# Kernel tuning notes

Measured on AMD Instinct MI355X. Metric: run time of the kernel, lower is better.

## Reference

```python
import jax, jax.numpy as jnp
import numpy as np

EPS = 1e-5

def _conv(x, w, b):
    # NCHW x OIHW -> NCHW, stride 1, SAME padding (stencil center (1,1) of 3x3, or 1x1)
    y = jax.lax.conv_general_dilated(x, w, (1, 1), 'SAME',
                                     dimension_numbers=('NCHW', 'OIHW', 'NCHW'))
    return y + b[None, :, None, None]

def _bn(x, gamma, beta):
    # training-mode batchnorm: stats over (N, H, W) per channel
    mean = jnp.mean(x, axis=(0, 2, 3), keepdims=True)
    var = jnp.var(x, axis=(0, 2, 3), keepdims=True)
    xhat = (x - mean) * jax.lax.rsqrt(var + EPS)
    return xhat * gamma[None, :, None, None] + beta[None, :, None, None]

def setup_inputs() -> dict:
    key = jax.random.key(0)
    ks = jax.random.split(key, 12)
    B, Cin, Cout, H, W = 2, 64, 64, 512, 512
    s = 0.05
    return {
        'x':  jax.random.normal(ks[0], (B, Cin, H, W), jnp.float32),
        'w1': jax.random.normal(ks[1], (Cout, Cin, 3, 3), jnp.float32) * s,
        'b1': jnp.zeros((Cout,), jnp.float32),
        'g1': jnp.ones((Cout,), jnp.float32),
        'be1': jnp.zeros((Cout,), jnp.float32),
        'w2': jax.random.normal(ks[2], (Cout, Cout, 3, 3), jnp.float32) * s,
        'b2': jnp.zeros((Cout,), jnp.float32),
        'g2': jnp.ones((Cout,), jnp.float32),
        'be2': jnp.zeros((Cout,), jnp.float32),
        'wp': jax.random.normal(ks[3], (Cout, Cin, 1, 1), jnp.float32) * s,
        'bp': jnp.zeros((Cout,), jnp.float32),
        'gp': jnp.ones((Cout,), jnp.float32),
        'bep': jnp.zeros((Cout,), jnp.float32),
    }

def reference(x, w1, b1, g1, be1, w2, b2, g2, be2, wp, bp, gp, bep):
    # project branch: 1x1 conv ([(0,0)] stencil) + BN
    residual = _bn(_conv(x, wp, bp), gp, bep)
    # conv1: pad + 3x3 lattice conv (full cp stencil) + BN + Identity downsample + ReLU
    out = jax.nn.relu(_bn(_conv(x, w1, b1), g1, be1))
    # conv2: pad + 3x3 lattice conv + BN
    out = _bn(_conv(out, w2, b2), g2, be2)
    # residual add + output ReLU
    return jax.nn.relu(out + residual)
```

## Files before the change

kernel.cpp:

```cpp
#include <hip/hip_runtime.h>
#include <hip/hip_bf16.h>
#include <stdint.h>

typedef short short8 __attribute__((ext_vector_type(8)));
typedef float f32x4 __attribute__((ext_vector_type(4)));
typedef unsigned int u32;
typedef unsigned short u16;

#define HH 512
#define WW 512
#define CC 64
#define PLANE (HH*WW)
#define NSTATF 524288.0f

#define KTW 32
#define HSTR 560
#define KBSTR 1120
#define SLOTB 4480
#define NSLOT 8
#define RINGB (NSLOT*SLOTB)
#define BOUNCEB 16384
#define NBC 1024
#define K5S 260

__device__ __forceinline__ u16 f2bf(float f) {
  __hip_bfloat16 h = __float2bfloat16(f);
  return __builtin_bit_cast(u16, h);
}
__device__ __forceinline__ u32 pk2bf(float a, float b) {
  return (u32)f2bf(a) | ((u32)f2bf(b) << 16);
}
__device__ __forceinline__ float bf2f(u16 u) {
  u32 x = ((u32)u) << 16;
  return __builtin_bit_cast(float, x);
}
__device__ __forceinline__ void lds_barrier() {
  asm volatile("s_waitcnt lgkmcnt(0)" ::: "memory");
  __builtin_amdgcn_s_barrier();
  __builtin_amdgcn_sched_barrier(0);
}

__global__ __launch_bounds__(512) void kprep(const float* __restrict__ w1,
    const float* __restrict__ w2, const float* __restrict__ wp,
    u16* __restrict__ wb1, u16* __restrict__ wb2, u16* __restrict__ wbp)
{
  const int id = blockIdx.x*512 + threadIdx.x;
  const int lane = id & 63;
  if (id < 9216) {
    const float* w = (id < 4608) ? w1 : w2;
    u16* o = (id < 4608) ? wb1 : wb2;
    const int fid = (id < 4608) ? (id >> 6) : ((id - 4608) >> 6);
    const int ct4 = fid / 18, rem = fid % 18;
    const int tap = rem >> 1, kb = rem & 1;
    const int cout = ct4*16 + (lane & 15);
    const int k0c = kb*32 + (lane >> 4)*8;
    u32 ow[4];
#pragma unroll
    for (int p = 0; p < 4; ++p) {
      float a = w[(size_t)(cout*64 + k0c + p*2    )*9 + tap];
      float b = w[(size_t)(cout*64 + k0c + p*2 + 1)*9 + tap];
      ow[p] = pk2bf(a, b);
    }
    *(uint4*)(o + ((size_t)fid*64 + lane)*8) = make_uint4(ow[0],ow[1],ow[2],ow[3]);
  } else if (id < 9728) {
    const int fid = (id - 9216) >> 6;
    const int ct4 = fid >> 1, kb = fid & 1;
    const int cout = ct4*16 + (lane & 15);
    const int k0c = kb*32 + (lane >> 4)*8;
    u32 ow[4];
#pragma unroll
    for (int p = 0; p < 4; ++p)
      ow[p] = pk2bf(wp[cout*64 + k0c + p*2], wp[cout*64 + k0c + p*2 + 1]);
    *(uint4*)(wbp + ((size_t)fid*64 + lane)*8) = make_uint4(ow[0],ow[1],ow[2],ow[3]);
  }
}

__global__ __launch_bounds__(256) void k0(const float* __restrict__ x, u16* __restrict__ xh)
{
  __shared__ __align__(16) u32 Tp[32*260];
  const int tid = threadIdx.x;
  const int wt = blockIdx.x, h = blockIdx.y, n = blockIdx.z;
  const int w0 = wt*256;
  const float* xp = x + (size_t)n*CC*PLANE + (size_t)h*WW + w0;
#pragma unroll
  for (int it = 0; it < 8; ++it) {
    const int j = it*256 + tid;
    const int c2 = j >> 6, w4 = (j & 63) << 2;
    const f32x4 a = *(const f32x4*)(xp + (size_t)(c2*2    )*PLANE + w4);
    const f32x4 b = *(const f32x4*)(xp + (size_t)(c2*2 + 1)*PLANE + w4);
    uint4 o;
    o.x = pk2bf(a[0], b[0]);
    o.y = pk2bf(a[1], b[1]);
    o.z = pk2bf(a[2], b[2]);
    o.w = pk2bf(a[3], b[3]);
    *(uint4*)(Tp + (u32)c2*260 + (u32)(w4 ^ (4*(c2 >> 2)))) = o;
  }
  __syncthreads();
  u16* op = xh + ((size_t)(n*HH + h)*WW + w0)*CC;
#pragma unroll
  for (int it = 0; it < 8; ++it) {
    const int j = it*256 + tid;
    const int w = j >> 3, c8 = j & 7;
    const u32 wsw = (u32)(w ^ (4*c8));
    uint4 o;
    o.x = Tp[(u32)(c8*4 + 0)*260 + wsw];
    o.y = Tp[(u32)(c8*4 + 1)*260 + wsw];
    o.z = Tp[(u32)(c8*4 + 2)*260 + wsw];
    o.w = Tp[(u32)(c8*4 + 3)*260 + wsw];
    *(uint4*)(op + (size_t)w*CC + c8*8) = o;
  }
}

template<bool BNS, bool PROJ>
__global__ __launch_bounds__(256, 2) void kconv(const u16* __restrict__ in,
    const u16* __restrict__ wb, const u16* __restrict__ wbp,
    const float* __restrict__ As, const float* __restrict__ Bs,
    u16* __restrict__ out, u16* __restrict__ yp,
    float* __restrict__ ps, float* __restrict__ pq,
    float* __restrict__ psp, float* __restrict__ pqp)
{
  __shared__ __align__(16) char LB[RINGB + BOUNCEB + 512];
  float* sA = (float*)(LB + RINGB + BOUNCEB);
  float* sB = sA + 64;
  const int tid = threadIdx.x;
  const int lane = tid & 63, wv = tid >> 6;
  const int l15 = lane & 15, lq = lane >> 4;
  const int wt = blockIdx.x, hs = blockIdx.y, n = blockIdx.z;
  const int w0 = wt*KTW, h0 = hs*16;
  const int bid = (n*32 + hs)*16 + wt;

  if (BNS) {
    if (tid < 64) { sA[tid] = As[tid]; sB[tid] = Bs[tid]; }
    __syncthreads();
  }

  short8 wfr[18];
#pragma unroll
  for (int f = 0; f < 18; ++f)
    wfr[f] = *(const short8*)(wb + ((size_t)(wv*18 + f)*64 + lane)*8);
  short8 wpf[2];
  if constexpr (PROJ) {
#pragma unroll
    for (int kb = 0; kb < 2; ++kb)
      wpf[kb] = *(const short8*)(wbp + ((size_t)(wv*2 + kb)*64 + lane)*8);
  }

  float s4[4] = {0,0,0,0}, q4[4] = {0,0,0,0};
  float sp4[4] = {0,0,0,0}, qp4[4] = {0,0,0,0};
  const u16* inb = in + (size_t)n*PLANE*CC;
  const u32 co0 = (u32)((lq >> 1)*KBSTR + (lq & 1)*HSTR);
  const u32 co1 = co0 + 2*KBSTR;

  auto ld_one = [&](int j, int cl, int c8) -> uint4 {
    const int gh = h0 - 1 + j, gw = w0 - 1 + cl;
    if (((u32)gh < (u32)HH) && ((u32)gw < (u32)WW))
      return *(const uint4*)(inb + ((size_t)gh*WW + gw)*CC + c8*8);
    return make_uint4(0u,0u,0u,0u);
  };
  auto st_one = [&](int slot, int cl, int c8, uint4 v) {
    if (BNS) {
      const u32* uw = (const u32*)&v;
      u32 ow[4];
      const int cb = c8*8;
#pragma unroll
      for (int h2 = 0; h2 < 4; ++h2) {
        float f0 = fmaxf(bf2f((u16)(uw[h2] & 0xFFFFu)) * sA[cb+h2*2]   + sB[cb+h2*2],   0.f);
        float f1 = fmaxf(bf2f((u16)(uw[h2] >> 16))     * sA[cb+h2*2+1] + sB[cb+h2*2+1], 0.f);
        ow[h2] = pk2bf(f0, f1);
      }
      v = make_uint4(ow[0],ow[1],ow[2],ow[3]);
    }
    *(uint4*)(LB + (size_t)slot*SLOTB + (c8>>1)*KBSTR + (c8&1)*HSTR + cl*16) = v;
  };

  for (int idx = tid; idx < 4*272; idx += 256) {
    const int jj = idx / 272, rem = idx - jj*272;
    st_one(jj, rem >> 3, rem & 7, ld_one(jj, rem >> 3, rem & 7));
  }
  __syncthreads();

  uint4 st0, st1, st2;
  auto issue2 = [&](int jb) {
    { const int idx = tid;       const int jj = idx/272, rem = idx - jj*272;
      st0 = ld_one(jb + jj, rem >> 3, rem & 7); }
    { const int idx = 256 + tid; const int jj = idx/272, rem = idx - jj*272;
      st1 = ld_one(jb + jj, rem >> 3, rem & 7); }
    if (tid < 32) { const int idx = 512 + tid; const int jj = idx/272, rem = idx - jj*272;
      st2 = ld_one(jb + jj, rem >> 3, rem & 7); }
  };
  auto write2 = [&](int jb) {
    { const int idx = tid;       const int jj = idx/272, rem = idx - jj*272;
      st_one((jb + jj) & 7, rem >> 3, rem & 7, st0); }
    { const int idx = 256 + tid; const int jj = idx/272, rem = idx - jj*272;
      st_one((jb + jj) & 7, rem >> 3, rem & 7, st1); }
    if (tid < 32) { const int idx = 512 + tid; const int jj = idx/272, rem = idx - jj*272;
      st_one((jb + jj) & 7, rem >> 3, rem & 7, st2); }
  };

  issue2(4);

  for (int g = 0; g < 8; ++g) {
    if (g > 0) write2(2*g + 2);
    lds_barrier();
    if (g < 7) issue2(2*g + 4);

    const char* sb[4];
#pragma unroll
    for (int mi = 0; mi < 4; ++mi)
      sb[mi] = LB + (size_t)((2*g + mi) & 7)*SLOTB + l15*16;
    f32x4 a0t0, a0t1, a1t0, a1t1;
    f32x4 p0t0, p0t1, p1t0, p1t1;
#pragma unroll
    for (int r = 0; r < 4; ++r) {
      a0t0[r]=0.f; a0t1[r]=0.f; a1t0[r]=0.f; a1t1[r]=0.f;
      p0t0[r]=0.f; p0t1[r]=0.f; p1t0[r]=0.f; p1t1[r]=0.f;
    }
#pragma unroll
    for (int t = 0; t < 2; ++t) {
      const int pb = t*16;
#pragma unroll
      for (int kb = 0; kb < 2; ++kb) {
        const u32 ck = kb ? co1 : co0;
#pragma unroll
        for (int mi = 0; mi < 4; ++mi) {
#pragma unroll
          for (int kw = 0; kw < 3; ++kw) {
            const short8 X = *(const short8*)(sb[mi] + ck + (u32)((pb + kw)*16));
            if (mi <= 2) {
              const short8 Wf = wfr[(mi*3 + kw)*2 + kb];
              if (t == 0) a0t0 = __builtin_amdgcn_mfma_f32_16x16x32_bf16(Wf, X, a0t0, 0,0,0);
              else        a0t1 = __builtin_amdgcn_mfma_f32_16x16x32_bf16(Wf, X, a0t1, 0,0,0);
            }
            if (mi >= 1) {
              const short8 Wf = wfr[((mi-1)*3 + kw)*2 + kb];
              if (t == 0) a1t0 = __builtin_amdgcn_mfma_f32_16x16x32_bf16(Wf, X, a1t0, 0,0,0);
              else        a1t1 = __builtin_amdgcn_mfma_f32_16x16x32_bf16(Wf, X, a1t1, 0,0,0);
            }
            if constexpr (PROJ) {
              if (kw == 1 && mi == 1) {
                if (t == 0) p0t0 = __builtin_amdgcn_mfma_f32_16x16x32_bf16(wpf[kb], X, p0t0, 0,0,0);
                else        p0t1 = __builtin_amdgcn_mfma_f32_16x16x32_bf16(wpf[kb], X, p0t1, 0,0,0);
              }
              if (kw == 1 && mi == 2) {
                if (t == 0) p1t0 = __builtin_amdgcn_mfma_f32_16x16x32_bf16(wpf[kb], X, p1t0, 0,0,0);
                else        p1t1 = __builtin_amdgcn_mfma_f32_16x16x32_bf16(wpf[kb], X, p1t1, 0,0,0);
              }
            }
          }
        }
      }
    }
    {
      const int co = wv*16 + lq*4;
#pragma unroll
      for (int r = 0; r < 4; ++r) {
        s4[r] += a0t0[r] + a0t1[r] + a1t0[r] + a1t1[r];
        q4[r] = fmaf(a0t0[r], a0t0[r], q4[r]);
        q4[r] = fmaf(a0t1[r], a0t1[r], q4[r]);
        q4[r] = fmaf(a1t0[r], a1t0[r], q4[r]);
        q4[r] = fmaf(a1t1[r], a1t1[r], q4[r]);
      }
      if constexpr (PROJ) {
#pragma unroll
        for (int r = 0; r < 4; ++r) {
          sp4[r] += p0t0[r] + p0t1[r] + p1t0[r] + p1t1[r];
          qp4[r] = fmaf(p0t0[r], p0t0[r], qp4[r]);
          qp4[r] = fmaf(p0t1[r], p0t1[r], qp4[r]);
          qp4[r] = fmaf(p1t0[r], p1t0[r], qp4[r]);
          qp4[r] = fmaf(p1t1[r], p1t1[r], qp4[r]);
        }
      }
#pragma unroll
      for (int t = 0; t < 2; ++t) {
        const int pos = t*16 + l15;
        const u32 addr = ((u32)(pos*128 + co*2)) ^ (((u32)(pos & 7)) << 4);
        uint2 c0, c1;
        if (t == 0) {
          c0.x = pk2bf(a0t0[0], a0t0[1]); c0.y = pk2bf(a0t0[2], a0t0[3]);
          c1.x = pk2bf(a1t0[0], a1t0[1]); c1.y = pk2bf(a1t0[2], a1t0[3]);
        } else {
          c0.x = pk2bf(a0t1[0], a0t1[1]); c0.y = pk2bf(a0t1[2], a0t1[3]);
          c1.x = pk2bf(a1t1[0], a1t1[1]); c1.y = pk2bf(a1t1[2], a1t1[3]);
        }
        *(uint2*)(LB + RINGB + 0*4096 + addr) = c0;
        *(uint2*)(LB + RINGB + 1*4096 + addr) = c1;
        if constexpr (PROJ) {
          uint2 d0, d1;
          if (t == 0) {
            d0.x = pk2bf(p0t0[0], p0t0[1]); d0.y = pk2bf(p0t0[2], p0t0[3]);
            d1.x = pk2bf(p1t0[0], p1t0[1]); d1.y = pk2bf(p1t0[2], p1t0[3]);
          } else {
            d0.x = pk2bf(p0t1[0], p0t1[1]); d0.y = pk2bf(p0t1[2], p0t1[3]);
            d1.x = pk2bf(p1t1[0], p1t1[1]); d1.y = pk2bf(p1t1[2], p1t1[3]);
          }
          *(uint2*)(LB + RINGB + 2*4096 + addr) = d0;
          *(uint2*)(LB + RINGB + 3*4096 + addr) = d1;
        }
      }
    }
    lds_barrier();
    if constexpr (PROJ) {
      const int rowi = tid >> 6, tt = tid & 63;
      const int pos = tt >> 1, half = (tt & 1)*64;
      const char* bb = LB + RINGB + rowi*4096;
      u16* base = (rowi < 2) ? out : yp;
      const int orow = h0 + 2*g + (rowi & 1);
      char* dst = (char*)base + ((size_t)((n*HH + orow)*WW + w0 + pos))*128 + half;
      const u32 sw = ((u32)(pos & 7)) << 4;
#pragma unroll
      for (int k2 = 0; k2 < 4; ++k2) {
        const uint4 v = *(const uint4*)(bb + (((u32)(pos*128 + half + k2*16)) ^ sw));
        *(uint4*)(dst + k2*16) = v;
      }
    } else {
      const int rowi = tid >> 7, tt = tid & 127;
      const int pos = tt >> 2, qb = (tt & 3)*32;
      const char* bb = LB + RINGB + rowi*4096;
      const u32 a0 = ((u32)(pos*128 + qb)) ^ (((u32)(pos & 7)) << 4);
      const uint4 v0 = *(const uint4*)(bb + a0);
      const uint4 v1 = *(const uint4*)(bb + (a0 ^ 16u));
      char* dst = (char*)out + ((size_t)((n*HH + h0 + 2*g + rowi)*WW + w0 + pos))*128 + qb;
      *(uint4*)dst = v0;
      *(uint4*)(dst + 16) = v1;
    }
  }

#pragma unroll
  for (int d = 1; d <= 8; d <<= 1) {
#pragma unroll
    for (int r = 0; r < 4; ++r) {
      s4[r] += __shfl_xor(s4[r], d, 64);
      q4[r] += __shfl_xor(q4[r], d, 64);
    }
  }
  if (l15 == 0) {
#pragma unroll
    for (int r = 0; r < 4; ++r) {
      const int co = wv*16 + lq*4 + r;
      ps[(size_t)co*NBC + bid] = s4[r];
      pq[(size_t)co*NBC + bid] = q4[r];
    }
  }
  if constexpr (PROJ) {
#pragma unroll
    for (int d = 1; d <= 8; d <<= 1) {
#pragma unroll
      for (int r = 0; r < 4; ++r) {
        sp4[r] += __shfl_xor(sp4[r], d, 64);
        qp4[r] += __shfl_xor(qp4[r], d, 64);
      }
    }
    if (l15 == 0) {
#pragma unroll
      for (int r = 0; r < 4; ++r) {
        const int co = wv*16 + lq*4 + r;
        psp[(size_t)co*NBC + bid] = sp4[r];
        pqp[(size_t)co*NBC + bid] = qp4[r];
      }
    }
  }
}

__global__ __launch_bounds__(256) void kfin2(
    const float* __restrict__ psA, const float* __restrict__ pqA,
    const float* __restrict__ gA, const float* __restrict__ beA,
    float* __restrict__ AA, float* __restrict__ BA, int cntA,
    const float* __restrict__ psB, const float* __restrict__ pqB,
    const float* __restrict__ gB, const float* __restrict__ beB,
    float* __restrict__ AB, float* __restrict__ BB, int cntB)
{
  const int blk = blockIdx.x;
  const bool second = blk >= 64;
  const int c = blk & 63;
  const float* psx = second ? psB : psA;
  const float* pqx = second ? pqB : pqA;
  const float* g  = second ? gB  : gA;
  const float* be = second ? beB : beA;
  float* A  = second ? AB : AA;
  float* Bc = second ? BB : BA;
  const int cnt = second ? cntB : cntA;

  const int t = threadIdx.x;
  float sv = 0.f, s2 = 0.f;
  const float* pr = psx + (size_t)c*cnt;
  const float* qr = pqx + (size_t)c*cnt;
  for (int k = t; k < cnt; k += 256) { sv += pr[k]; s2 += qr[k]; }
#pragma unroll
  for (int d = 1; d < 64; d <<= 1) { sv += __shfl_xor(sv, d, 64); s2 += __shfl_xor(s2, d, 64); }
  __shared__ float as_[4], aq_[4];
  if ((t & 63) == 0) { as_[t >> 6] = sv; aq_[t >> 6] = s2; }
  __syncthreads();
  if (t == 0) {
    sv = as_[0] + as_[1] + as_[2] + as_[3];
    s2 = aq_[0] + aq_[1] + aq_[2] + aq_[3];
    const float mean = sv / NSTATF;
    const float var = s2 / NSTATF - mean*mean;
    const float istd = rsqrtf(var + 1e-5f);
    const float a = g[c] * istd;
    A[c] = a;
    Bc[c] = be[c] - mean * a;
  }
}

__global__ __launch_bounds__(256) void k5(const u16* __restrict__ y2, const u16* __restrict__ yp,
    const float* __restrict__ A2, const float* __restrict__ B2c,
    const float* __restrict__ Ap, const float* __restrict__ Bp,
    float* __restrict__ outp)
{
  __shared__ float T[CC*K5S];
  __shared__ float cA2[64], cB2[64], cAp[64], cBp[64];
  const int tid = threadIdx.x;
  const int lane = tid & 63, wv = tid >> 6;
  const int wt = blockIdx.x, h = blockIdx.y, n = blockIdx.z;
  const int w0 = wt*256;
  if (tid < 64) { cA2[tid] = A2[tid]; cB2[tid] = B2c[tid]; cAp[tid] = Ap[tid]; cBp[tid] = Bp[tid]; }
  __syncthreads();
  const u16* p2 = y2 + ((size_t)(n*HH + h)*WW + w0)*CC;
  const u16* pp = yp + ((size_t)(n*HH + h)*WW + w0)*CC;
#pragma unroll
  for (int it = 0; it < 8; ++it) {
    const int j = it*256 + tid;
    const int w = j >> 3, c8 = j & 7;
    const uint4 u2 = *(const uint4*)(p2 + (size_t)w*CC + c8*8);
    const uint4 up = *(const uint4*)(pp + (size_t)w*CC + c8*8);
    const u32* m2 = (const u32*)&u2;
    const u32* mp = (const u32*)&up;
    const u32 sw = ((u32)(c8 & 3)) << 3;
#pragma unroll
    for (int h2 = 0; h2 < 4; ++h2) {
      const int c = c8*8 + h2*2;
      const float a = bf2f((u16)(m2[h2] & 0xFFFFu)), b = bf2f((u16)(m2[h2] >> 16));
      const float ra = bf2f((u16)(mp[h2] & 0xFFFFu)), rb = bf2f((u16)(mp[h2] >> 16));
      const u32 wsw = (u32)w ^ sw;
      T[(u32)(c    )*K5S + wsw] = fmaxf(a*cA2[c]   + cB2[c]   + ra*cAp[c]   + cBp[c],   0.f);
      T[(u32)(c + 1)*K5S + wsw] = fmaxf(b*cA2[c+1] + cB2[c+1] + rb*cAp[c+1] + cBp[c+1], 0.f);
    }
  }
  __syncthreads();
#pragma unroll
  for (int cc = 0; cc < 16; ++cc) {
    const int c = cc*4 + wv;
    const u32 sw = ((u32)((c >> 3) & 3)) << 3;
    const u32 idx = (u32)c*K5S + (((u32)lane*4) ^ sw);
    const f32x4 v = *(const f32x4*)(T + idx);
    *(f32x4*)(outp + ((size_t)((n*CC + c)*HH + h))*WW + w0 + lane*4) = v;
  }
}

extern "C" void kernel_launch(void* const* d_in, const int* in_sizes, int n_in,
                              void* d_out, int out_size, void* d_ws, size_t ws_size,
                              hipStream_t stream)
{
  (void)in_sizes; (void)n_in; (void)out_size;
  const float* x   = (const float*)d_in[0];
  const float* w1  = (const float*)d_in[1];
  const float* g1  = (const float*)d_in[3];
  const float* be1 = (const float*)d_in[4];
  const float* w2  = (const float*)d_in[5];
  const float* g2  = (const float*)d_in[7];
  const float* be2 = (const float*)d_in[8];
  const float* wp  = (const float*)d_in[9];
  const float* gp  = (const float*)d_in[11];
  const float* bep = (const float*)d_in[12];

  const size_t TENB = (size_t)2*CC*PLANE*2;
  char* ws = (char*)d_ws;
  u16* bufA = (u16*)ws;
  u16* bufB = (u16*)(ws + TENB);
  u16* bufC = (u16*)(ws + TENB*2);
  char* aux = ws + TENB*3;
  u16* wb1 = (u16*)aux;
  u16* wb2 = (u16*)(aux + 73728);
  u16* wbp = (u16*)(aux + 147456);
  float* ps1 = (float*)(aux + 155648);
  float* pq1 = ps1 + 64*NBC;
  float* ps2 = pq1 + 64*NBC;
  float* pq2 = ps2 + 64*NBC;
  float* psp = pq2 + 64*NBC;
  float* pqp = psp + 64*NBC;
  float* A1  = pqp + 64*NBC;
  float* B1  = A1 + 64;
  float* A2  = B1 + 64;
  float* B2c = A2 + 64;
  float* Ap  = B2c + 64;
  float* Bp  = Ap + 64;
  const size_t need = (size_t)(Bp + 64 - (float*)ws) * 4;
  if (ws_size < need) return;

  kprep<<<19, 512, 0, stream>>>(w1, w2, wp, wb1, wb2, wbp);
  k0<<<dim3(2, HH, 2), 256, 0, stream>>>(x, bufA);
  kconv<false, true><<<dim3(16, 32, 2), 256, 0, stream>>>(bufA, wb1, wbp, nullptr, nullptr,
                                                          bufB, bufC, ps1, pq1, psp, pqp);
  kfin2<<<128, 256, 0, stream>>>(ps1, pq1, g1, be1, A1, B1, NBC,
                                 psp, pqp, gp, bep, Ap, Bp, NBC);
  kconv<true, false><<<dim3(16, 32, 2), 256, 0, stream>>>(bufB, wb2, nullptr, A1, B1,
                                                          bufA, nullptr, ps2, pq2, nullptr, nullptr);
  kfin2<<<64, 256, 0, stream>>>(ps2, pq2, g2, be2, A2, B2c, NBC,
                                ps2, pq2, g2, be2, A2, B2c, NBC);
  k5<<<dim3(2, HH, 2), 256, 0, stream>>>(bufA, bufC, A2, B2c, Ap, Bp, (float*)d_out);
}
```

Baseline: 223.5 us.

## Rewrite second conv with 32x32 MFMA tiles and deeper staging ring

Splits the templated conv kernel into a specialised conv1 (with fused projection) and a new conv2. Conv2 uses 32x32x16 bf16 MFMA with each wave owning 32 output channels and two output rows, and a 10-slot LDS ring staging four rows per step. The goal is better MFMA throughput and fewer barrier steps per block. It costs more registers, since 36 weight fragments and 16-wide accumulators are held per wave, which may hurt occupancy. The final epilogue kernel also moves to half-width tiles, doubling its grid and using float2 stores.

```diff
diff --git a/kernel.cpp b/kernel.cpp
--- a/kernel.cpp
+++ b/kernel.cpp
@@ -4,6 +4,7 @@
 
 typedef short short8 __attribute__((ext_vector_type(8)));
 typedef float f32x4 __attribute__((ext_vector_type(4)));
+typedef float f32x16 __attribute__((ext_vector_type(16)));
 typedef unsigned int u32;
 typedef unsigned short u16;
 
@@ -14,14 +15,19 @@
 #define NSTATF 524288.0f
 
 #define KTW 32
-#define HSTR 560
-#define KBSTR 1120
-#define SLOTB 4480
-#define NSLOT 8
-#define RINGB (NSLOT*SLOTB)
+#define HSTR1 560
+#define KBSTR1 1120
+#define SLOTB1 4480
+#define RING1 (8*SLOTB1)
+#define HSTR2 592
+#define KBSTR2 1184
+#define SLOTB2 4736
+#define NSLOT2 10
+#define RING2 (NSLOT2*SLOTB2)
 #define BOUNCEB 16384
-#define NBC 1024
-#define K5S 260
+#define NBC1 1024
+#define NBC2 2048
+#define K5S 132
 
 __device__ __forceinline__ u16 f2bf(float f) {
   __hip_bfloat16 h = __float2bfloat16(f);
@@ -46,10 +52,8 @@
 {
   const int id = blockIdx.x*512 + threadIdx.x;
   const int lane = id & 63;
-  if (id < 9216) {
-    const float* w = (id < 4608) ? w1 : w2;
-    u16* o = (id < 4608) ? wb1 : wb2;
-    const int fid = (id < 4608) ? (id >> 6) : ((id - 4608) >> 6);
+  if (id < 4608) {
+    const int fid = id >> 6;
     const int ct4 = fid / 18, rem = fid % 18;
     const int tap = rem >> 1, kb = rem & 1;
     const int cout = ct4*16 + (lane & 15);
@@ -57,11 +61,23 @@
     u32 ow[4];
 #pragma unroll
     for (int p = 0; p < 4; ++p) {
-      float a = w[(size_t)(cout*64 + k0c + p*2    )*9 + tap];
-      float b = w[(size_t)(cout*64 + k0c + p*2 + 1)*9 + tap];
-      ow[p] = pk2bf(a, b);
-    }
-    *(uint4*)(o + ((size_t)fid*64 + lane)*8) = make_uint4(ow[0],ow[1],ow[2],ow[3]);
+      ow[p] = pk2bf(w1[(size_t)(cout*64 + k0c + p*2)*9 + tap],
+                    w1[(size_t)(cout*64 + k0c + p*2 + 1)*9 + tap]);
+    }
+    *(uint4*)(wb1 + ((size_t)fid*64 + lane)*8) = make_uint4(ow[0],ow[1],ow[2],ow[3]);
+  } else if (id < 9216) {
+    const int fid = (id - 4608) >> 6;
+    const int ct = fid / 36, rem = fid % 36;
+    const int tap = rem >> 2, kb = rem & 3;
+    const int cout = ct*32 + (lane & 31);
+    const int cinb = kb*16 + (lane >> 5)*8;
+    u32 ow[4];
+#pragma unroll
+    for (int p = 0; p < 4; ++p) {
+      ow[p] = pk2bf(w2[(size_t)(cout*64 + cinb + p*2)*9 + tap],
+                    w2[(size_t)(cout*64 + cinb + p*2 + 1)*9 + tap]);
+    }
+    *(uint4*)(wb2 + ((size_t)fid*64 + lane)*8) = make_uint4(ow[0],ow[1],ow[2],ow[3]);
   } else if (id < 9728) {
     const int fid = (id - 9216) >> 6;
     const int ct4 = fid >> 1, kb = fid & 1;
@@ -111,17 +127,13 @@
   }
 }
 
-template<bool BNS, bool PROJ>
-__global__ __launch_bounds__(256, 2) void kconv(const u16* __restrict__ in,
+__global__ __launch_bounds__(256, 2) void kconv1(const u16* __restrict__ in,
     const u16* __restrict__ wb, const u16* __restrict__ wbp,
-    const float* __restrict__ As, const float* __restrict__ Bs,
     u16* __restrict__ out, u16* __restrict__ yp,
     float* __restrict__ ps, float* __restrict__ pq,
     float* __restrict__ psp, float* __restrict__ pqp)
 {
-  __shared__ __align__(16) char LB[RINGB + BOUNCEB + 512];
-  float* sA = (float*)(LB + RINGB + BOUNCEB);
-  float* sB = sA + 64;
+  __shared__ __align__(16) char LB[RING1 + BOUNCEB + 512];
   const int tid = threadIdx.x;
   const int lane = tid & 63, wv = tid >> 6;
   const int l15 = lane & 15, lq = lane >> 4;
@@ -129,27 +141,20 @@
   const int w0 = wt*KTW, h0 = hs*16;
   const int bid = (n*32 + hs)*16 + wt;
 
-  if (BNS) {
-    if (tid < 64) { sA[tid] = As[tid]; sB[tid] = Bs[tid]; }
-    __syncthreads();
-  }
-
   short8 wfr[18];
 #pragma unroll
   for (int f = 0; f < 18; ++f)
     wfr[f] = *(const short8*)(wb + ((size_t)(wv*18 + f)*64 + lane)*8);
   short8 wpf[2];
-  if constexpr (PROJ) {
-#pragma unroll
-    for (int kb = 0; kb < 2; ++kb)
-      wpf[kb] = *(const short8*)(wbp + ((size_t)(wv*2 + kb)*64 + lane)*8);
-  }
+#pragma unroll
+  for (int kb = 0; kb < 2; ++kb)
+    wpf[kb] = *(const short8*)(wbp + ((size_t)(wv*2 + kb)*64 + lane)*8);
 
   float s4[4] = {0,0,0,0}, q4[4] = {0,0,0,0};
   float sp4[4] = {0,0,0,0}, qp4[4] = {0,0,0,0};
   const u16* inb = in + (size_t)n*PLANE*CC;
-  const u32 co0 = (u32)((lq >> 1)*KBSTR + (lq & 1)*HSTR);
-  const u32 co1 = co0 + 2*KBSTR;
+  const u32 co0 = (u32)((lq >> 1)*KBSTR1 + (lq & 1)*HSTR1);
+  const u32 co1 = co0 + 2*KBSTR1;
 
   auto ld_one = [&](int j, int cl, int c8) -> uint4 {
     const int gh = h0 - 1 + j, gw = w0 - 1 + cl;
@@ -158,19 +163,7 @@
     return make_uint4(0u,0u,0u,0u);
   };
   auto st_one = [&](int slot, int cl, int c8, uint4 v) {
-    if (BNS) {
-      const u32* uw = (const u32*)&v;
-      u32 ow[4];
-      const int cb = c8*8;
-#pragma unroll
-      for (int h2 = 0; h2 < 4; ++h2) {
-        float f0 = fmaxf(bf2f((u16)(uw[h2] & 0xFFFFu)) * sA[cb+h2*2]   + sB[cb+h2*2],   0.f);
-        float f1 = fmaxf(bf2f((u16)(uw[h2] >> 16))     * sA[cb+h2*2+1] + sB[cb+h2*2+1], 0.f);
-        ow[h2] = pk2bf(f0, f1);
-      }
-      v = make_uint4(ow[0],ow[1],ow[2],ow[3]);
-    }
-    *(uint4*)(LB + (size_t)slot*SLOTB + (c8>>1)*KBSTR + (c8&1)*HSTR + cl*16) = v;
+    *(uint4*)(LB + (size_t)slot*SLOTB1 + (c8>>1)*KBSTR1 + (c8&1)*HSTR1 + cl*16) = v;
   };
 
   for (int idx = tid; idx < 4*272; idx += 256) {
@@ -207,7 +200,7 @@
     const char* sb[4];
 #pragma unroll
     for (int mi = 0; mi < 4; ++mi)
-      sb[mi] = LB + (size_t)((2*g + mi) & 7)*SLOTB + l15*16;
+      sb[mi] = LB + (size_t)((2*g + mi) & 7)*SLOTB1 + l15*16;
     f32x4 a0t0, a0t1, a1t0, a1t1;
     f32x4 p0t0, p0t1, p1t0, p1t1;
 #pragma unroll
@@ -236,15 +229,13 @@
               if (t == 0) a1t0 = __builtin_amdgcn_mfma_f32_16x16x32_bf16(Wf, X, a1t0, 0,0,0);
               else        a1t1 = __builtin_amdgcn_mfma_f32_16x16x32_bf16(Wf, X, a1t1, 0,0,0);
             }
-            if constexpr (PROJ) {
-              if (kw == 1 && mi == 1) {
-                if (t == 0) p0t0 = __builtin_amdgcn_mfma_f32_16x16x32_bf16(wpf[kb], X, p0t0, 0,0,0);
-                else        p0t1 = __builtin_amdgcn_mfma_f32_16x16x32_bf16(wpf[kb], X, p0t1, 0,0,0);
-              }
-              if (kw == 1 && mi == 2) {
-                if (t == 0) p1t0 = __builtin_amdgcn_mfma_f32_16x16x32_bf16(wpf[kb], X, p1t0, 0,0,0);
-                else        p1t1 = __builtin_amdgcn_mfma_f32_16x16x32_bf16(wpf[kb], X, p1t1, 0,0,0);
-              }
+            if (kw == 1 && mi == 1) {
+              if (t == 0) p0t0 = __builtin_amdgcn_mfma_f32_16x16x32_bf16(wpf[kb], X, p0t0, 0,0,0);
+              else        p0t1 = __builtin_amdgcn_mfma_f32_16x16x32_bf16(wpf[kb], X, p0t1, 0,0,0);
+            }
+            if (kw == 1 && mi == 2) {
+              if (t == 0) p1t0 = __builtin_amdgcn_mfma_f32_16x16x32_bf16(wpf[kb], X, p1t0, 0,0,0);
+              else        p1t1 = __builtin_amdgcn_mfma_f32_16x16x32_bf16(wpf[kb], X, p1t1, 0,0,0);
             }
           }
         }
@@ -259,50 +250,39 @@
         q4[r] = fmaf(a0t1[r], a0t1[r], q4[r]);
         q4[r] = fmaf(a1t0[r], a1t0[r], q4[r]);
         q4[r] = fmaf(a1t1[r], a1t1[r], q4[r]);
-      }
-      if constexpr (PROJ) {
-#pragma unroll
-        for (int r = 0; r < 4; ++r) {
-          sp4[r] += p0t0[r] + p0t1[r] + p1t0[r] + p1t1[r];
-          qp4[r] = fmaf(p0t0[r], p0t0[r], qp4[r]);
-          qp4[r] = fmaf(p0t1[r], p0t1[r], qp4[r]);
-          qp4[r] = fmaf(p1t0[r], p1t0[r], qp4[r]);
-          qp4[r] = fmaf(p1t1[r], p1t1[r], qp4[r]);
-        }
+        sp4[r] += p0t0[r] + p0t1[r] + p1t0[r] + p1t1[r];
+        qp4[r] = fmaf(p0t0[r], p0t0[r], qp4[r]);
+        qp4[r] = fmaf(p0t1[r], p0t1[r], qp4[r]);
+        qp4[r] = fmaf(p1t0[r], p1t0[r], qp4[r]);
+        qp4[r] = fmaf(p1t1[r], p1t1[r], qp4[r]);
       }
 #pragma unroll
       for (int t = 0; t < 2; ++t) {
         const int pos = t*16 + l15;
         const u32 addr = ((u32)(pos*128 + co*2)) ^ (((u32)(pos & 7)) << 4);
-        uint2 c0, c1;
+        uint2 c0, c1, d0, d1;
         if (t == 0) {
           c0.x = pk2bf(a0t0[0], a0t0[1]); c0.y = pk2bf(a0t0[2], a0t0[3]);
           c1.x = pk2bf(a1t0[0], a1t0[1]); c1.y = pk2bf(a1t0[2], a1t0[3]);
+          d0.x = pk2bf(p0t0[0], p0t0[1]); d0.y = pk2bf(p0t0[2], p0t0[3]);
+          d1.x = pk2bf(p1t0[0], p1t0[1]); d1.y = pk2bf(p1t0[2], p1t0[3]);
         } else {
           c0.x = pk2bf(a0t1[0], a0t1[1]); c0.y = pk2bf(a0t1[2], a0t1[3]);
           c1.x = pk2bf(a1t1[0], a1t1[1]); c1.y = pk2bf(a1t1[2], a1t1[3]);
+          d0.x = pk2bf(p0t1[0], p0t1[1]); d0.y = pk2bf(p0t1[2], p0t1[3]);
+          d1.x = pk2bf(p1t1[0], p1t1[1]); d1.y = pk2bf(p1t1[2], p1t1[3]);
         }
-        *(uint2*)(LB + RINGB + 0*4096 + addr) = c0;
-        *(uint2*)(LB + RINGB + 1*4096 + addr) = c1;
-        if constexpr (PROJ) {
-          uint2 d0, d1;
-          if (t == 0) {
-            d0.x = pk2bf(p0t0[0], p0t0[1]); d0.y = pk2bf(p0t0[2], p0t0[3]);
-            d1.x = pk2bf(p1t0[0], p1t0[1]); d1.y = pk2bf(p1t0[2], p1t0[3]);
-          } else {
-            d0.x = pk2bf(p0t1[0], p0t1[1]); d0.y = pk2bf(p0t1[2], p0t1[3]);
-            d1.x = pk2bf(p1t1[0], p1t1[1]); d1.y = pk2bf(p1t1[2], p1t1[3]);
-          }
-          *(uint2*)(LB + RINGB + 2*4096 + addr) = d0;
-          *(uint2*)(LB + RINGB + 3*4096 + addr) = d1;
-        }
+        *(uint2*)(LB + RING1 + 0*4096 + addr) = c0;
+        *(uint2*)(LB + RING1 + 1*4096 + addr) = c1;
+        *(uint2*)(LB + RING1 + 2*4096 + addr) = d0;
+        *(uint2*)(LB + RING1 + 3*4096 + addr) = d1;
       }
     }
     lds_barrier();
-    if constexpr (PROJ) {
+    {
       const int rowi = tid >> 6, tt = tid & 63;
       const int pos = tt >> 1, half = (tt & 1)*64;
-      const char* bb = LB + RINGB + rowi*4096;
+      const char* bb = LB + RING1 + rowi*4096;
       u16* base = (rowi < 2) ? out : yp;
       const int orow = h0 + 2*g + (rowi & 1);
       char* dst = (char*)base + ((size_t)((n*HH + orow)*WW + w0 + pos))*128 + half;
@@ -312,16 +292,6 @@
         const uint4 v = *(const uint4*)(bb + (((u32)(pos*128 + half + k2*16)) ^ sw));
         *(uint4*)(dst + k2*16) = v;
       }
-    } else {
-      const int rowi = tid >> 7, tt = tid & 127;
-      const int pos = tt >> 2, qb = (tt & 3)*32;
-      const char* bb = LB + RINGB + rowi*4096;
-      const u32 a0 = ((u32)(pos*128 + qb)) ^ (((u32)(pos & 7)) << 4);
-      const uint4 v0 = *(const uint4*)(bb + a0);
-      const uint4 v1 = *(const uint4*)(bb + (a0 ^ 16u));
-      char* dst = (char*)out + ((size_t)((n*HH + h0 + 2*g + rowi)*WW + w0 + pos))*128 + qb;
-      *(uint4*)dst = v0;
-      *(uint4*)(dst + 16) = v1;
     }
   }
 
@@ -331,32 +301,190 @@
     for (int r = 0; r < 4; ++r) {
       s4[r] += __shfl_xor(s4[r], d, 64);
       q4[r] += __shfl_xor(q4[r], d, 64);
+      sp4[r] += __shfl_xor(sp4[r], d, 64);
+      qp4[r] += __shfl_xor(qp4[r], d, 64);
     }
   }
   if (l15 == 0) {
 #pragma unroll
     for (int r = 0; r < 4; ++r) {
       const int co = wv*16 + lq*4 + r;
-      ps[(size_t)co*NBC + bid] = s4[r];
-      pq[(size_t)co*NBC + bid] = q4[r];
-    }
-  }
-  if constexpr (PROJ) {
-#pragma unroll
-    for (int d = 1; d <= 8; d <<= 1) {
-#pragma unroll
-      for (int r = 0; r < 4; ++r) {
-        sp4[r] += __shfl_xor(sp4[r], d, 64);
-        qp4[r] += __shfl_xor(qp4[r], d, 64);
-      }
-    }
-    if (l15 == 0) {
-#pragma unroll
-      for (int r = 0; r < 4; ++r) {
-        const int co = wv*16 + lq*4 + r;
-        psp[(size_t)co*NBC + bid] = sp4[r];
-        pqp[(size_t)co*NBC + bid] = qp4[r];
-      }
+      ps[(size_t)co*NBC1 + bid] = s4[r];
+      pq[(size_t)co*NBC1 + bid] = q4[r];
+      psp[(size_t)co*NBC1 + bid] = sp4[r];
+      pqp[(size_t)co*NBC1 + bid] = qp4[r];
+    }
+  }
+}
+
+__global__ __launch_bounds__(256, 2) void kconv2(const u16* __restrict__ in,
+    const u16* __restrict__ wb,
+    const float* __restrict__ As, const float* __restrict__ Bs,
+    u16* __restrict__ out, float* __restrict__ ps, float* __restrict__ pq)
+{
+  __shared__ __align__(16) char LB[RING2 + BOUNCEB + 512];
+  float* sA = (float*)(LB + RING2 + BOUNCEB);
+  float* sB = sA + 64;
+  const int tid = threadIdx.x;
+  const int lane = tid & 63, wv = tid >> 6;
+  const int ct = wv & 1, ro = wv >> 1;
+  const int wt = blockIdx.x, hs = blockIdx.y, n = blockIdx.z;
+  const int w0 = wt*KTW, h0 = hs*16;
+  const int bid = (n*32 + hs)*16 + wt;
+
+  if (tid < 64) { sA[tid] = As[tid]; sB[tid] = Bs[tid]; }
+  __syncthreads();
+
+  short8 wfr[36];
+#pragma unroll
+  for (int f = 0; f < 36; ++f)
+    wfr[f] = *(const short8*)(wb + ((size_t)(ct*36 + f)*64 + lane)*8);
+  float s[16], q[16];
+#pragma unroll
+  for (int r = 0; r < 16; ++r) { s[r] = 0.f; q[r] = 0.f; }
+
+  const u16* inb = in + (size_t)n*PLANE*CC;
+  const u32 lt = (u32)((lane & 31)*16 + (lane >> 5)*HSTR2);
+
+  auto ld_one = [&](int j, int cl, int c8) -> uint4 {
+    const int gh = h0 - 1 + j, gw = w0 - 1 + cl;
+    if (((u32)gh < (u32)HH) && ((u32)gw < (u32)WW))
+      return *(const uint4*)(inb + ((size_t)gh*WW + gw)*CC + c8*8);
+    return make_uint4(0u,0u,0u,0u);
+  };
+  auto st_one = [&](int slot, int cl, int c8, uint4 v) {
+    const u32* uw = (const u32*)&v;
+    u32 ow[4];
+    const int cb = c8*8;
+#pragma unroll
+    for (int h2 = 0; h2 < 4; ++h2) {
+      float f0 = fmaxf(bf2f((u16)(uw[h2] & 0xFFFFu)) * sA[cb+h2*2]   + sB[cb+h2*2],   0.f);
+      float f1 = fmaxf(bf2f((u16)(uw[h2] >> 16))     * sA[cb+h2*2+1] + sB[cb+h2*2+1], 0.f);
+      ow[h2] = pk2bf(f0, f1);
+    }
+    *(uint4*)(LB + (size_t)slot*SLOTB2 + (c8>>1)*KBSTR2 + (c8&1)*HSTR2 + cl*16) =
+        make_uint4(ow[0],ow[1],ow[2],ow[3]);
+  };
+
+  for (int idx = tid; idx < 6*272; idx += 256) {
+    const int jj = idx / 272, rem = idx - jj*272;
+    st_one(jj, rem >> 3, rem & 7, ld_one(jj, rem >> 3, rem & 7));
+  }
+  __syncthreads();
+
+  for (int g = 0; g < 4; ++g) {
+    const bool dostage = (g <= 2);
+    const int jb = 4*g + 6;
+    uint4 st0, st1, st2, st3, st4;
+    if (dostage) {
+      { const int idx = tid;        const int jj = idx/272, rem = idx - jj*272;
+        st0 = ld_one(jb + jj, rem >> 3, rem & 7); }
+      { const int idx = 256 + tid;  const int jj = idx/272, rem = idx - jj*272;
+        st1 = ld_one(jb + jj, rem >> 3, rem & 7); }
+      { const int idx = 512 + tid;  const int jj = idx/272, rem = idx - jj*272;
+        st2 = ld_one(jb + jj, rem >> 3, rem & 7); }
+      { const int idx = 768 + tid;  const int jj = idx/272, rem = idx - jj*272;
+        st3 = ld_one(jb + jj, rem >> 3, rem & 7); }
+      if (tid < 64) { const int idx = 1024 + tid; const int jj = idx/272, rem = idx - jj*272;
+        st4 = ld_one(jb + jj, rem >> 3, rem & 7); }
+    }
+
+    const int r0 = 4*g + 2*ro;
+    f32x16 acc0, acc1;
+#pragma unroll
+    for (int rr = 0; rr < 16; ++rr) { acc0[rr] = 0.f; acc1[rr] = 0.f; }
+    {
+      const char* bm[4];
+#pragma unroll
+      for (int mi = 0; mi < 4; ++mi) {
+        int sl = r0 + mi; if (sl >= NSLOT2) sl -= NSLOT2;
+        bm[mi] = LB + (size_t)sl*SLOTB2 + lt;
+      }
+#pragma unroll
+      for (int kb = 0; kb < 4; ++kb) {
+#pragma unroll
+        for (int mi = 0; mi < 4; ++mi) {
+          const char* bp_ = bm[mi] + kb*KBSTR2;
+#pragma unroll
+          for (int kw = 0; kw < 3; ++kw) {
+            const short8 X = *(const short8*)(bp_ + kw*16);
+            if (mi <= 2)
+              acc0 = __builtin_amdgcn_mfma_f32_32x32x16_bf16(wfr[(mi*3+kw)*4+kb], X, acc0, 0,0,0);
+            if (mi >= 1)
+              acc1 = __builtin_amdgcn_mfma_f32_32x32x16_bf16(wfr[((mi-1)*3+kw)*4+kb], X, acc1, 0,0,0);
+          }
+        }
+      }
+    }
+    {
+      const int pos = lane & 31;
+      const int cob = ct*32 + 4*(lane>>5);
+#pragma unroll
+      for (int rr = 0; rr < 16; ++rr) {
+        const float v0 = acc0[rr], v1 = acc1[rr];
+        s[rr] += v0 + v1;
+        q[rr] = fmaf(v0, v0, q[rr]);
+        q[rr] = fmaf(v1, v1, q[rr]);
+      }
+#pragma unroll
+      for (int k = 0; k < 4; ++k) {
+        const u32 addr = ((u32)(pos*128 + (cob + 8*k)*2)) ^ (((u32)(pos & 7)) << 4);
+        uint2 p0, p1;
+        p0.x = pk2bf(acc0[4*k],   acc0[4*k+1]);
+        p0.y = pk2bf(acc0[4*k+2], acc0[4*k+3]);
+        p1.x = pk2bf(acc1[4*k],   acc1[4*k+1]);
+        p1.y = pk2bf(acc1[4*k+2], acc1[4*k+3]);
+        *(uint2*)(LB + RING2 + (2*ro    )*4096 + addr) = p0;
+        *(uint2*)(LB + RING2 + (2*ro + 1)*4096 + addr) = p1;
+      }
+    }
+    lds_barrier();
+    {
+      const int rowi = tid >> 6, tt = tid & 63;
+      const int pos = tt >> 1, half = (tt & 1)*64;
+      const char* bb = LB + RING2 + rowi*4096;
+      char* dst = (char*)out + ((size_t)((n*HH + h0 + 4*g + rowi)*WW + w0 + pos))*128 + half;
+      const u32 sw = ((u32)(pos & 7)) << 4;
+#pragma unroll
+      for (int k2 = 0; k2 < 4; ++k2) {
+        const uint4 v = *(const uint4*)(bb + (((u32)(pos*128 + half + k2*16)) ^ sw));
+        *(uint4*)(dst + k2*16) = v;
+      }
+    }
+    if (dostage) {
+      { const int idx = tid;        const int jj = idx/272, rem = idx - jj*272;
+        int sl = jb + jj; if (sl >= NSLOT2) sl -= NSLOT2;
+        st_one(sl, rem >> 3, rem & 7, st0); }
+      { const int idx = 256 + tid;  const int jj = idx/272, rem = idx - jj*272;
+        int sl = jb + jj; if (sl >= NSLOT2) sl -= NSLOT2;
+        st_one(sl, rem >> 3, rem & 7, st1); }
+      { const int idx = 512 + tid;  const int jj = idx/272, rem = idx - jj*272;
+        int sl = jb + jj; if (sl >= NSLOT2) sl -= NSLOT2;
+        st_one(sl, rem >> 3, rem & 7, st2); }
+      { const int idx = 768 + tid;  const int jj = idx/272, rem = idx - jj*272;
+        int sl = jb + jj; if (sl >= NSLOT2) sl -= NSLOT2;
+        st_one(sl, rem >> 3, rem & 7, st3); }
+      if (tid < 64) { const int idx = 1024 + tid; const int jj = idx/272, rem = idx - jj*272;
+        int sl = jb + jj; if (sl >= NSLOT2) sl -= NSLOT2;
+        st_one(sl, rem >> 3, rem & 7, st4); }
+    }
+    lds_barrier();
+  }
+
+#pragma unroll
+  for (int d = 1; d <= 16; d <<= 1) {
+#pragma unroll
+    for (int rr = 0; rr < 16; ++rr) {
+      s[rr] += __shfl_xor(s[rr], d, 64);
+      q[rr] += __shfl_xor(q[rr], d, 64);
+    }
+  }
+  if ((lane & 31) == 0) {
+#pragma unroll
+    for (int rr = 0; rr < 16; ++rr) {
+      const int co = ct*32 + (rr&3) + 8*(rr>>2) + 4*(lane>>5);
+      ps[(size_t)co*NBC2 + bid*2 + ro] = s[rr];
+      pq[(size_t)co*NBC2 + bid*2 + ro] = q[rr];
     }
   }
 }
@@ -412,13 +540,13 @@
   const int tid = threadIdx.x;
   const int lane = tid & 63, wv = tid >> 6;
   const int wt = blockIdx.x, h = blockIdx.y, n = blockIdx.z;
-  const int w0 = wt*256;
+  const int w0 = wt*128;
   if (tid < 64) { cA2[tid] = A2[tid]; cB2[tid] = B2c[tid]; cAp[tid] = Ap[tid]; cBp[tid] = Bp[tid]; }
   __syncthreads();
   const u16* p2 = y2 + ((size_t)(n*HH + h)*WW + w0)*CC;
   const u16* pp = yp + ((size_t)(n*HH + h)*WW + w0)*CC;
 #pragma unroll
-  for (int it = 0; it < 8; ++it) {
+  for (int it = 0; it < 4; ++it) {
     const int j = it*256 + tid;
     const int w = j >> 3, c8 = j & 7;
     const uint4 u2 = *(const uint4*)(p2 + (size_t)w*CC + c8*8);
@@ -441,9 +569,11 @@
   for (int cc = 0; cc < 16; ++cc) {
     const int c = cc*4 + wv;
     const u32 sw = ((u32)((c >> 3) & 3)) << 3;
-    const u32 idx = (u32)c*K5S + (((u32)lane*4) ^ sw);
-    const f32x4 v = *(const f32x4*)(T + idx);
-    *(f32x4*)(outp + ((size_t)((n*CC + c)*HH + h))*WW + w0 + lane*4) = v;
+    const u32 idx = (u32)c*K5S + (((u32)(lane*2)) ^ sw);
+    float2 v;
+    v.x = T[idx];
+    v.y = T[idx + 1];
+    *(float2*)(outp + ((size_t)((n*CC + c)*HH + h))*WW + w0 + lane*2) = v;
   }
 }
 
@@ -473,12 +603,12 @@
   u16* wb2 = (u16*)(aux + 73728);
   u16* wbp = (u16*)(aux + 147456);
   float* ps1 = (float*)(aux + 155648);
-  float* pq1 = ps1 + 64*NBC;
-  float* ps2 = pq1 + 64*NBC;
-  float* pq2 = ps2 + 64*NBC;
-  float* psp = pq2 + 64*NBC;
-  float* pqp = psp + 64*NBC;
-  float* A1  = pqp + 64*NBC;
+  float* pq1 = ps1 + 64*NBC1;
+  float* psp = pq1 + 64*NBC1;
+  float* pqp = psp + 64*NBC1;
+  float* ps2 = pqp + 64*NBC1;
+  float* pq2 = ps2 + 64*NBC2;
+  float* A1  = pq2 + 64*NBC2;
   float* B1  = A1 + 64;
   float* A2  = B1 + 64;
   float* B2c = A2 + 64;
@@ -489,13 +619,13 @@
 
   kprep<<<19, 512, 0, stream>>>(w1, w2, wp, wb1, wb2, wbp);
   k0<<<dim3(2, HH, 2), 256, 0, stream>>>(x, bufA);
-  kconv<false, true><<<dim3(16, 32, 2), 256, 0, stream>>>(bufA, wb1, wbp, nullptr, nullptr,
-                                                          bufB, bufC, ps1, pq1, psp, pqp);
-  kfin2<<<128, 256, 0, stream>>>(ps1, pq1, g1, be1, A1, B1, NBC,
-                                 psp, pqp, gp, bep, Ap, Bp, NBC);
-  kconv<true, false><<<dim3(16, 32, 2), 256, 0, stream>>>(bufB, wb2, nullptr, A1, B1,
-                                                          bufA, nullptr, ps2, pq2, nullptr, nullptr);
-  kfin2<<<64, 256, 0, stream>>>(ps2, pq2, g2, be2, A2, B2c, NBC,
-                                ps2, pq2, g2, be2, A2, B2c, NBC);
-  k5<<<dim3(2, HH, 2), 256, 0, stream>>>(bufA, bufC, A2, B2c, Ap, Bp, (float*)d_out);
-}
+  kconv1<<<dim3(16, 32, 2), 256, 0, stream>>>(bufA, wb1, wbp,
+                                              bufB, bufC, ps1, pq1, psp, pqp);
+  kfin2<<<128, 256, 0, stream>>>(ps1, pq1, g1, be1, A1, B1, NBC1,
+                                 psp, pqp, gp, bep, Ap, Bp, NBC1);
+  kconv2<<<dim3(16, 32, 2), 256, 0, stream>>>(bufB, wb2, A1, B1,
+                                              bufA, ps2, pq2);
+  kfin2<<<64, 256, 0, stream>>>(ps2, pq2, g2, be2, A2, B2c, NBC2,
+                                ps2, pq2, g2, be2, A2, B2c, NBC2);
+  k5<<<dim3(4, HH, 2), 256, 0, stream>>>(bufA, bufC, A2, B2c, Ap, Bp, (float*)d_out);
+}
```

Result: slower. 249.1 us (+11.5%).
